# Performance work log

Measured on AMD Instinct MI355X. Metric: run time of the kernel, lower is better.

The kernel has to match this reference:

```python
import jax, jax.numpy as jnp
import numpy as np

IN_C, HID_C, OUT_C = 256, 512, 256
B, N = 8, 4096


def setup_inputs() -> dict:
    key = jax.random.key(0)
    ks = jax.random.split(key, 6)
    x = jax.random.normal(ks[0], (B, N, IN_C), dtype=jnp.float32)
    A = jax.random.uniform(ks[1], (B, N, N), dtype=jnp.float32)
    # Glorot-ish init for the two GCN layer weights + zero biases (PyG default bias=True)
    W1 = jax.random.normal(ks[2], (IN_C, HID_C), dtype=jnp.float32) * (1.0 / np.sqrt(IN_C))
    b1 = jnp.zeros((HID_C,), dtype=jnp.float32)
    W2 = jax.random.normal(ks[3], (HID_C, OUT_C), dtype=jnp.float32) * (1.0 / np.sqrt(HID_C))
    b2 = jnp.zeros((OUT_C,), dtype=jnp.float32)
    return {"x": x, "A": A, "W1": W1, "b1": b1, "W2": W2, "b2": b2}


def _gcn_norm(A):
    # dense equivalent of PyG gcn_norm with add_self_loops: A_hat = A + I,
    # norm = D^{-1/2} A_hat D^{-1/2}, with deg==0 -> 0 (inf guarded)
    A_hat = A + jnp.eye(A.shape[-1], dtype=A.dtype)  # [B,N,N]
    deg = A_hat.sum(axis=-1)                          # [B,N]
    d_inv_sqrt = jnp.where(deg > 0, jax.lax.rsqrt(jnp.maximum(deg, 1e-12)), 0.0)
    return d_inv_sqrt[:, :, None] * A_hat * d_inv_sqrt[:, None, :]


def reference(x, A, W1, b1, W2, b2):
    nrm = _gcn_norm(A)  # [B,N,N]
    # layer 1: out = A_hat_norm @ (x W1) + b1, then ReLU (dropout is identity in eval)
    h = jax.nn.relu(jnp.einsum('bij,bjh->bih', nrm, x @ W1) + b1)
    # layer 2
    out = jnp.einsum('bij,bjo->bio', nrm, h @ W2) + b2
    return out
```

## Files before the change

### kernel.cpp

```cpp
#include <hip/hip_runtime.h>
#include <stdint.h>

#define NN   4096
#define BATCH 8
#define IC   256
#define HC   512
#define OC   256
#define MTOT (BATCH * NN)

typedef float    f32x4 __attribute__((ext_vector_type(4)));
typedef __bf16   bf16x8 __attribute__((ext_vector_type(8)));
typedef uint16_t u16x8 __attribute__((ext_vector_type(8)));

__device__ __forceinline__ uint16_t f2b(float f) {
  union { float f; uint32_t u; } v; v.f = f;
  return (uint16_t)((v.u + 0x7FFFu + ((v.u >> 16) & 1u)) >> 16);
}

__global__ __launch_bounds__(256) void deg_kernel(const float* __restrict__ A,
                                                  float* __restrict__ dinv) {
  const int row = blockIdx.x;
  const float* ap = A + (size_t)row * NN;
  const int t = threadIdx.x;
  float s = 0.f;
#pragma unroll
  for (int i = 0; i < 4; ++i) {
    f32x4 v = *(const f32x4*)(ap + (t + 256 * i) * 4);
    s += v[0] + v[1] + v[2] + v[3];
  }
#pragma unroll
  for (int off = 32; off > 0; off >>= 1) s += __shfl_xor(s, off, 64);
  __shared__ float red[4];
  if ((t & 63) == 0) red[t >> 6] = s;
  __syncthreads();
  if (t == 0) {
    float deg = red[0] + red[1] + red[2] + red[3] + 1.0f;
    dinv[row] = 1.0f / sqrtf(deg);
  }
}

template<bool ABF16, int KTOT, int NC>
__global__ __launch_bounds__(256, 2) void xw_kernel(const void* __restrict__ Av,
                                                    const float* __restrict__ W,
                                                    const float* __restrict__ dinv,
                                                    uint16_t* __restrict__ Cout) {
  constexpr int BM = 128, BN = 128, BK = 64, LDT = 72;
  __shared__ uint16_t as_[BM * LDT];
  __shared__ uint16_t wt_[BN * LDT];
  const int t = threadIdx.x;
  const int m0 = blockIdx.x * BM;
  const int n0 = blockIdx.y * BN;
  const int lane = t & 63, wid = t >> 6;
  const int wm = wid >> 1, wn = wid & 1;
  f32x4 acc[4][4] = {};

  for (int kt = 0; kt < KTOT / BK; ++kt) {
    const int k0 = kt * BK;
    __syncthreads();
    if constexpr (!ABF16) {
      const float* Ap = (const float*)Av;
      const int c4 = t & 15, r0 = t >> 4;
#pragma unroll
      for (int i = 0; i < 8; ++i) {
        int r = r0 + 16 * i;
        f32x4 v = *(const f32x4*)(Ap + (size_t)(m0 + r) * KTOT + k0 + c4 * 4);
        uint32_t lo = f2b(v[0]) | ((uint32_t)f2b(v[1]) << 16);
        uint32_t hi = f2b(v[2]) | ((uint32_t)f2b(v[3]) << 16);
        *(uint2*)&as_[r * LDT + c4 * 4] = make_uint2(lo, hi);
      }
    } else {
      const uint16_t* Ap = (const uint16_t*)Av;
      const int c8 = t & 7, r0 = t >> 3;
#pragma unroll
      for (int i = 0; i < 4; ++i) {
        int r = r0 + 32 * i;
        u16x8 v = *(const u16x8*)(Ap + (size_t)(m0 + r) * KTOT + k0 + c8 * 8);
        *(u16x8*)&as_[r * LDT + c8 * 8] = v;
      }
    }
    {
      const int n4 = t & 31, kq = t >> 5;
#pragma unroll
      for (int i = 0; i < 8; ++i) {
        int k = kq + 8 * i;
        f32x4 v = *(const f32x4*)(W + (size_t)(k0 + k) * NC + n0 + n4 * 4);
        uint16_t hv[4] = { f2b(v[0]), f2b(v[1]), f2b(v[2]), f2b(v[3]) };
#pragma unroll
        for (int w = 0; w < 4; ++w) {
          int we = (w + n4) & 3;
          wt_[(n4 * 4 + we) * LDT + k] = hv[we];
        }
      }
    }
    __syncthreads();
#pragma unroll
    for (int kk = 0; kk < 2; ++kk) {
      bf16x8 bfr[4], afr[4];
#pragma unroll
      for (int fn = 0; fn < 4; ++fn)
        bfr[fn] = *(const bf16x8*)&wt_[(wn * 64 + fn * 16 + (lane & 15)) * LDT + kk * 32 + (lane >> 4) * 8];
#pragma unroll
      for (int fm = 0; fm < 4; ++fm)
        afr[fm] = *(const bf16x8*)&as_[(wm * 64 + fm * 16 + (lane & 15)) * LDT + kk * 32 + (lane >> 4) * 8];
#pragma unroll
      for (int fm = 0; fm < 4; ++fm)
#pragma unroll
        for (int fn = 0; fn < 4; ++fn)
          acc[fm][fn] = __builtin_amdgcn_mfma_f32_16x16x32_bf16(afr[fm], bfr[fn], acc[fm][fn], 0, 0, 0);
    }
  }
#pragma unroll
  for (int fm = 0; fm < 4; ++fm)
#pragma unroll
    for (int r = 0; r < 4; ++r) {
      int row = m0 + wm * 64 + fm * 16 + (lane >> 4) * 4 + r;
      float dv = dinv[row];
#pragma unroll
      for (int fn = 0; fn < 4; ++fn) {
        int col = n0 + wn * 64 + fn * 16 + (lane & 15);
        Cout[(size_t)row * NC + col] = f2b(acc[fm][fn][r] * dv);
      }
    }
}

template<int BN_, bool RELU>
__global__ __launch_bounds__(512, 2) void agg_kernel(const float* __restrict__ Amat,
                                                     const uint16_t* __restrict__ Vin,
                                                     const float* __restrict__ dinv,
                                                     const float* __restrict__ bias,
                                                     uint16_t* __restrict__ Hout,
                                                     float* __restrict__ Fout) {
  constexpr int BM = 128, BK = 64, LDT = 72;
  constexpr int FN = BN_ / 64;
  constexpr int WN = BN_ / 4;
  constexpr int CHN = BN_ / 8;
  constexpr int VT_TASKS = (64 * CHN) / 512;
  constexpr int NT = NN / BK;

  __shared__ uint16_t as_[BM * LDT];
  __shared__ uint16_t vt_[BN_ * LDT];

  const int t = threadIdx.x;
  const int bid = blockIdx.x;
  const int b = bid & 7;
  const int m0 = (bid >> 3) * BM;
  const int lane = t & 63, wid = t >> 6;
  const int wm = wid >> 2, wn = wid & 3;

  const float* Abase = Amat + ((size_t)b * NN + m0) * NN;
  const uint16_t* Vbase = Vin + (size_t)b * NN * BN_;

  const int ac4 = t & 15, ar0 = t >> 4;
  f32x4 apre[4];
  u16x8 vpre[VT_TASKS];

  auto load_tile = [&](int kt) {
    const int jj = kt * BK;
#pragma unroll
    for (int i = 0; i < 4; ++i)
      apre[i] = *(const f32x4*)(Abase + (size_t)(ar0 + 32 * i) * NN + jj + ac4 * 4);
#pragma unroll
    for (int i = 0; i < VT_TASKS; ++i) {
      int tt = i * 512 + t;
      int chunk = tt & (CHN - 1);
      int j = tt / CHN;
      vpre[i] = *(const u16x8*)(Vbase + (size_t)(jj + j) * BN_ + chunk * 8);
    }
  };

  load_tile(0);
  f32x4 acc[4][FN] = {};

  for (int kt = 0; kt < NT; ++kt) {
    const int j0 = kt * BK;
    __syncthreads();
#pragma unroll
    for (int i = 0; i < 4; ++i) {
      int r = ar0 + 32 * i;
      float f0 = apre[i][0], f1 = apre[i][1], f2c = apre[i][2], f3 = apre[i][3];
      int gc = j0 + ac4 * 4;
      int gr = m0 + r;
      if (gr == gc)          f0 += 1.0f;
      else if (gr == gc + 1) f1 += 1.0f;
      else if (gr == gc + 2) f2c += 1.0f;
      else if (gr == gc + 3) f3 += 1.0f;
      uint32_t lo = f2b(f0) | ((uint32_t)f2b(f1) << 16);
      uint32_t hi = f2b(f2c) | ((uint32_t)f2b(f3) << 16);
      *(uint2*)&as_[r * LDT + ac4 * 4] = make_uint2(lo, hi);
    }
#pragma unroll
    for (int i = 0; i < VT_TASKS; ++i) {
      int tt = i * 512 + t;
      int chunk = tt & (CHN - 1);
      int j = tt / CHN;
#pragma unroll
      for (int e = 0; e < 8; ++e) {
        int ee = (e + chunk) & 7;
        vt_[(chunk * 8 + ee) * LDT + j] = vpre[i][ee];
      }
    }
    __syncthreads();
    if (kt + 1 < NT) load_tile(kt + 1);
#pragma unroll
    for (int kk = 0; kk < 2; ++kk) {
      bf16x8 bfr[FN], afr[4];
#pragma unroll
      for (int fn = 0; fn < FN; ++fn)
        bfr[fn] = *(const bf16x8*)&vt_[(wn * WN + fn * 16 + (lane & 15)) * LDT + kk * 32 + (lane >> 4) * 8];
#pragma unroll
      for (int fm = 0; fm < 4; ++fm)
        afr[fm] = *(const bf16x8*)&as_[(wm * 64 + fm * 16 + (lane & 15)) * LDT + kk * 32 + (lane >> 4) * 8];
#pragma unroll
      for (int fm = 0; fm < 4; ++fm)
#pragma unroll
        for (int fn = 0; fn < FN; ++fn)
          acc[fm][fn] = __builtin_amdgcn_mfma_f32_16x16x32_bf16(afr[fm], bfr[fn], acc[fm][fn], 0, 0, 0);
    }
  }
#pragma unroll
  for (int fm = 0; fm < 4; ++fm)
#pragma unroll
    for (int r = 0; r < 4; ++r) {
      int rowl = wm * 64 + fm * 16 + (lane >> 4) * 4 + r;
      int grow = b * NN + m0 + rowl;
      float dv = dinv[grow];
#pragma unroll
      for (int fn = 0; fn < FN; ++fn) {
        int col = wn * WN + fn * 16 + (lane & 15);
        float v = acc[fm][fn][r] * dv + bias[col];
        if constexpr (RELU) {
          v = fmaxf(v, 0.0f);
          Hout[(size_t)grow * BN_ + col] = f2b(v);
        } else {
          Fout[(size_t)grow * BN_ + col] = v;
        }
      }
    }
}

extern "C" void kernel_launch(void* const* d_in, const int* in_sizes, int n_in,
                              void* d_out, int out_size, void* d_ws, size_t ws_size,
                              hipStream_t stream) {
  const float* x  = (const float*)d_in[0];
  const float* A  = (const float*)d_in[1];
  const float* W1 = (const float*)d_in[2];
  const float* b1 = (const float*)d_in[3];
  const float* W2 = (const float*)d_in[4];
  const float* b2 = (const float*)d_in[5];
  float* out = (float*)d_out;

  char* ws = (char*)d_ws;
  float*    dinv = (float*)ws;
  uint16_t* V1   = (uint16_t*)(ws + 131072);
  uint16_t* H    = (uint16_t*)(ws + 131072 + 33554432);
  uint16_t* V2   = (uint16_t*)(ws + 131072 + 2 * 33554432);

  deg_kernel<<<MTOT, 256, 0, stream>>>(A, dinv);
  xw_kernel<false, IC, HC><<<dim3(MTOT / 128, HC / 128), 256, 0, stream>>>(x, W1, dinv, V1);
  agg_kernel<HC, true><<<256, 512, 0, stream>>>(A, V1, dinv, b1, H, nullptr);
  xw_kernel<true, HC, OC><<<dim3(MTOT / 128, OC / 128), 256, 0, stream>>>(H, W2, dinv, V2);
  agg_kernel<OC, false><<<256, 512, 0, stream>>>(A, V2, dinv, b2, nullptr, out);
}
```

Baseline: 1.422 ms.

## Precompute normalized bf16 adjacency in tiled swizzled layout, load via global_load_lds

Adds a prep kernel that folds the self-loop and both D^-1/2 scalings into A once and stores it as bf16 in pre-tiled 64x64 XOR-swizzled blocks. The xw kernel now writes V transposed into the same tile layout, and the aggregation kernels stream both operands straight into LDS with global_load_lds, with no per-tile conversion or transpose. A is read in fp32 twice before this (degree plus prep) instead of three times, and each aggregation pass reads half the bytes of A. The cost is a 256 MB workspace and an extra pass that writes A. The aggregation tiles change to 64 rows by the full feature width, and the kernel no longer double-buffers its global loads.

```diff
diff --git a/kernel.cpp b/kernel.cpp
--- a/kernel.cpp
+++ b/kernel.cpp
@@ -6,15 +6,21 @@
 #define IC   256
 #define HC   512
 #define OC   256
-#define MTOT (BATCH * NN)
-
-typedef float    f32x4 __attribute__((ext_vector_type(4)));
+
+typedef float    f32x4  __attribute__((ext_vector_type(4)));
 typedef __bf16   bf16x8 __attribute__((ext_vector_type(8)));
-typedef uint16_t u16x8 __attribute__((ext_vector_type(8)));
+typedef uint16_t u16x8  __attribute__((ext_vector_type(8)));
+typedef uint16_t u16x4  __attribute__((ext_vector_type(4)));
 
 __device__ __forceinline__ uint16_t f2b(float f) {
   union { float f; uint32_t u; } v; v.f = f;
   return (uint16_t)((v.u + 0x7FFFu + ((v.u >> 16) & 1u)) >> 16);
+}
+
+__device__ __forceinline__ void gl_lds16(const void* g, void* l) {
+  __builtin_amdgcn_global_load_lds(
+      (const __attribute__((address_space(1))) uint32_t*)g,
+      (__attribute__((address_space(3))) uint32_t*)l, 16, 0, 0);
 }
 
 __global__ __launch_bounds__(256) void deg_kernel(const float* __restrict__ A,
@@ -39,23 +45,59 @@
   }
 }
 
+__global__ __launch_bounds__(256) void prep_kernel(const float* __restrict__ A,
+                                                   const float* __restrict__ dinv,
+                                                   uint16_t* __restrict__ Anorm) {
+  const int bid = blockIdx.x;
+  const int b = bid & 7, mt = (bid >> 3) & 63, kq = bid >> 9;
+  const int t = threadIdx.x;
+  const float* Ab = A + ((size_t)b * NN + mt * 64) * NN;
+  const float* dv = dinv + b * NN;
+  uint16_t* out = Anorm + ((size_t)(b * 64 + mt)) * 64 * 4096;
+  for (int kt = kq * 16; kt < kq * 16 + 16; ++kt) {
+#pragma unroll
+    for (int it = 0; it < 2; ++it) {
+      int tt = it * 256 + t;
+      int r = tt >> 3, g = tt & 7;
+      int i = mt * 64 + r;
+      int j0 = kt * 64 + g * 8;
+      const float* ap = Ab + (size_t)r * NN + j0;
+      f32x4 a0 = *(const f32x4*)ap;
+      f32x4 a1 = *(const f32x4*)(ap + 4);
+      float dvi = dv[i];
+      f32x4 d0 = *(const f32x4*)(dv + j0);
+      f32x4 d1 = *(const f32x4*)(dv + j0 + 4);
+      int dj = i - j0;
+      u16x8 o;
+#pragma unroll
+      for (int e = 0; e < 4; ++e) {
+        float v0 = (a0[e] + ((dj == e) ? 1.f : 0.f)) * dvi * d0[e];
+        float v1 = (a1[e] + ((dj == e + 4) ? 1.f : 0.f)) * dvi * d1[e];
+        o[e] = f2b(v0);
+        o[e + 4] = f2b(v1);
+      }
+      *(u16x8*)(out + ((size_t)kt * 64 + r) * 64 + (g ^ (r & 7)) * 8) = o;
+    }
+  }
+}
+
 template<bool ABF16, int KTOT, int NC>
 __global__ __launch_bounds__(256, 2) void xw_kernel(const void* __restrict__ Av,
                                                     const float* __restrict__ W,
-                                                    const float* __restrict__ dinv,
-                                                    uint16_t* __restrict__ Cout) {
-  constexpr int BM = 128, BN = 128, BK = 64, LDT = 72;
-  __shared__ uint16_t as_[BM * LDT];
-  __shared__ uint16_t wt_[BN * LDT];
-  const int t = threadIdx.x;
-  const int m0 = blockIdx.x * BM;
-  const int n0 = blockIdx.y * BN;
+                                                    uint16_t* __restrict__ Vt) {
+  constexpr int LDT = 72;
+  __shared__ uint16_t smem[18432];
+  uint16_t* as_ = smem;
+  uint16_t* wt_ = smem + 9216;
+  const int t = threadIdx.x;
+  const int m0 = blockIdx.x * 128;
+  const int n0 = blockIdx.y * 128;
   const int lane = t & 63, wid = t >> 6;
   const int wm = wid >> 1, wn = wid & 1;
   f32x4 acc[4][4] = {};
 
-  for (int kt = 0; kt < KTOT / BK; ++kt) {
-    const int k0 = kt * BK;
+  for (int kt = 0; kt < KTOT / 64; ++kt) {
+    const int k0 = kt * 64;
     __syncthreads();
     if constexpr (!ABF16) {
       const float* Ap = (const float*)Av;
@@ -109,111 +151,83 @@
           acc[fm][fn] = __builtin_amdgcn_mfma_f32_16x16x32_bf16(afr[fm], bfr[fn], acc[fm][fn], 0, 0, 0);
     }
   }
+  const int b = m0 >> 12;
+  const int kl0 = m0 & 4095;
+  __syncthreads();
+  uint16_t* lv = smem;
 #pragma unroll
   for (int fm = 0; fm < 4; ++fm)
 #pragma unroll
-    for (int r = 0; r < 4; ++r) {
-      int row = m0 + wm * 64 + fm * 16 + (lane >> 4) * 4 + r;
-      float dv = dinv[row];
-#pragma unroll
-      for (int fn = 0; fn < 4; ++fn) {
-        int col = n0 + wn * 64 + fn * 16 + (lane & 15);
-        Cout[(size_t)row * NC + col] = f2b(acc[fm][fn][r] * dv);
-      }
-    }
+    for (int fn = 0; fn < 4; ++fn) {
+      int nloc = wn * 64 + fn * 16 + (lane & 15);
+      int ml0  = wm * 64 + fm * 16 + (lane >> 4) * 4;
+      u16x4 pk;
+      pk[0] = f2b(acc[fm][fn][0]); pk[1] = f2b(acc[fm][fn][1]);
+      pk[2] = f2b(acc[fm][fn][2]); pk[3] = f2b(acc[fm][fn][3]);
+      *(u16x4*)&lv[nloc * 144 + ml0] = pk;
+    }
+  __syncthreads();
+#pragma unroll
+  for (int i = 0; i < 8; ++i) {
+    int nloc = (t >> 4) + 16 * i;
+    int ch = t & 15;
+    u16x8 v = *(const u16x8*)&lv[nloc * 144 + ch * 8];
+    int nglob = n0 + nloc;
+    int ktv = (kl0 >> 6) + (ch >> 3);
+    int s = (ch & 7) ^ (nglob & 7);
+    *(u16x8*)(Vt + (((size_t)b * 64 + ktv) * NC + nglob) * 64 + s * 8) = v;
+  }
 }
 
 template<int BN_, bool RELU>
-__global__ __launch_bounds__(512, 2) void agg_kernel(const float* __restrict__ Amat,
-                                                     const uint16_t* __restrict__ Vin,
-                                                     const float* __restrict__ dinv,
+__global__ __launch_bounds__(BN_, 4) void agg_kernel(const uint16_t* __restrict__ Anorm,
+                                                     const uint16_t* __restrict__ Vt,
                                                      const float* __restrict__ bias,
                                                      uint16_t* __restrict__ Hout,
                                                      float* __restrict__ Fout) {
-  constexpr int BM = 128, BK = 64, LDT = 72;
-  constexpr int FN = BN_ / 64;
-  constexpr int WN = BN_ / 4;
-  constexpr int CHN = BN_ / 8;
-  constexpr int VT_TASKS = (64 * CHN) / 512;
-  constexpr int NT = NN / BK;
-
-  __shared__ uint16_t as_[BM * LDT];
-  __shared__ uint16_t vt_[BN_ * LDT];
-
-  const int t = threadIdx.x;
+  constexpr int NWAVES = BN_ / 64;
+  __shared__ uint16_t as_[64 * 64];
+  __shared__ uint16_t vt_[BN_ * 64];
+  const int t = threadIdx.x;
+  const int lane = t & 63, wid = t >> 6;
   const int bid = blockIdx.x;
-  const int b = bid & 7;
-  const int m0 = (bid >> 3) * BM;
-  const int lane = t & 63, wid = t >> 6;
-  const int wm = wid >> 2, wn = wid & 3;
-
-  const float* Abase = Amat + ((size_t)b * NN + m0) * NN;
-  const uint16_t* Vbase = Vin + (size_t)b * NN * BN_;
-
-  const int ac4 = t & 15, ar0 = t >> 4;
-  f32x4 apre[4];
-  u16x8 vpre[VT_TASKS];
-
-  auto load_tile = [&](int kt) {
-    const int jj = kt * BK;
-#pragma unroll
-    for (int i = 0; i < 4; ++i)
-      apre[i] = *(const f32x4*)(Abase + (size_t)(ar0 + 32 * i) * NN + jj + ac4 * 4);
-#pragma unroll
-    for (int i = 0; i < VT_TASKS; ++i) {
-      int tt = i * 512 + t;
-      int chunk = tt & (CHN - 1);
-      int j = tt / CHN;
-      vpre[i] = *(const u16x8*)(Vbase + (size_t)(jj + j) * BN_ + chunk * 8);
-    }
-  };
-
-  load_tile(0);
-  f32x4 acc[4][FN] = {};
-
-  for (int kt = 0; kt < NT; ++kt) {
-    const int j0 = kt * BK;
-    __syncthreads();
-#pragma unroll
-    for (int i = 0; i < 4; ++i) {
-      int r = ar0 + 32 * i;
-      float f0 = apre[i][0], f1 = apre[i][1], f2c = apre[i][2], f3 = apre[i][3];
-      int gc = j0 + ac4 * 4;
-      int gr = m0 + r;
-      if (gr == gc)          f0 += 1.0f;
-      else if (gr == gc + 1) f1 += 1.0f;
-      else if (gr == gc + 2) f2c += 1.0f;
-      else if (gr == gc + 3) f3 += 1.0f;
-      uint32_t lo = f2b(f0) | ((uint32_t)f2b(f1) << 16);
-      uint32_t hi = f2b(f2c) | ((uint32_t)f2b(f3) << 16);
-      *(uint2*)&as_[r * LDT + ac4 * 4] = make_uint2(lo, hi);
-    }
-#pragma unroll
-    for (int i = 0; i < VT_TASKS; ++i) {
-      int tt = i * 512 + t;
-      int chunk = tt & (CHN - 1);
-      int j = tt / CHN;
-#pragma unroll
-      for (int e = 0; e < 8; ++e) {
-        int ee = (e + chunk) & 7;
-        vt_[(chunk * 8 + ee) * LDT + j] = vpre[i][ee];
-      }
-    }
-    __syncthreads();
-    if (kt + 1 < NT) load_tile(kt + 1);
+  const int b = bid & 7, mt = bid >> 3;
+  const int fr = lane & 15, c = lane >> 4;
+
+  const uint16_t* Abase = Anorm + ((size_t)(b * 64 + mt)) * 64 * 4096;
+  const uint16_t* Vbase = Vt + (size_t)b * 64 * BN_ * 64;
+
+  f32x4 acc[4][4] = {};
+
+  for (int kt = 0; kt < 64; ++kt) {
+    __syncthreads();
+    const uint16_t* At    = Abase + (size_t)kt * 4096;
+    const uint16_t* Vtile = Vbase + (size_t)kt * (BN_ * 64);
+    for (int ca = wid; ca < 8; ca += NWAVES)
+      gl_lds16(At + ca * 512 + lane * 8, &as_[ca * 512]);
+#pragma unroll
+    for (int i = 0; i < 8; ++i) {
+      int cv = wid * 8 + i;
+      gl_lds16(Vtile + cv * 512 + lane * 8, &vt_[cv * 512]);
+    }
+    __syncthreads();
 #pragma unroll
     for (int kk = 0; kk < 2; ++kk) {
-      bf16x8 bfr[FN], afr[4];
-#pragma unroll
-      for (int fn = 0; fn < FN; ++fn)
-        bfr[fn] = *(const bf16x8*)&vt_[(wn * WN + fn * 16 + (lane & 15)) * LDT + kk * 32 + (lane >> 4) * 8];
+      bf16x8 afr[4], bfr[4];
+#pragma unroll
+      for (int fm = 0; fm < 4; ++fm) {
+        int row = fm * 16 + fr;
+        afr[fm] = *(const bf16x8*)&as_[row * 64 + (((kk << 2) + c) ^ (row & 7)) * 8];
+      }
+#pragma unroll
+      for (int fn = 0; fn < 4; ++fn) {
+        int n = wid * 64 + fn * 16 + fr;
+        bfr[fn] = *(const bf16x8*)&vt_[n * 64 + (((kk << 2) + c) ^ (n & 7)) * 8];
+      }
 #pragma unroll
       for (int fm = 0; fm < 4; ++fm)
-        afr[fm] = *(const bf16x8*)&as_[(wm * 64 + fm * 16 + (lane & 15)) * LDT + kk * 32 + (lane >> 4) * 8];
-#pragma unroll
-      for (int fm = 0; fm < 4; ++fm)
-#pragma unroll
-        for (int fn = 0; fn < FN; ++fn)
+#pragma unroll
+        for (int fn = 0; fn < 4; ++fn)
           acc[fm][fn] = __builtin_amdgcn_mfma_f32_16x16x32_bf16(afr[fm], bfr[fn], acc[fm][fn], 0, 0, 0);
     }
   }
@@ -221,18 +235,15 @@
   for (int fm = 0; fm < 4; ++fm)
 #pragma unroll
     for (int r = 0; r < 4; ++r) {
-      int rowl = wm * 64 + fm * 16 + (lane >> 4) * 4 + r;
-      int grow = b * NN + m0 + rowl;
-      float dv = dinv[grow];
-#pragma unroll
-      for (int fn = 0; fn < FN; ++fn) {
-        int col = wn * WN + fn * 16 + (lane & 15);
-        float v = acc[fm][fn][r] * dv + bias[col];
+      size_t grow = (size_t)b * NN + mt * 64 + fm * 16 + (lane >> 4) * 4 + r;
+#pragma unroll
+      for (int fn = 0; fn < 4; ++fn) {
+        int col = wid * 64 + fn * 16 + fr;
+        float v = acc[fm][fn][r] + bias[col];
         if constexpr (RELU) {
-          v = fmaxf(v, 0.0f);
-          Hout[(size_t)grow * BN_ + col] = f2b(v);
+          Hout[grow * BN_ + col] = f2b(fmaxf(v, 0.f));
         } else {
-          Fout[(size_t)grow * BN_ + col] = v;
+          Fout[grow * BN_ + col] = v;
         }
       }
     }
@@ -250,14 +261,15 @@
   float* out = (float*)d_out;
 
   char* ws = (char*)d_ws;
-  float*    dinv = (float*)ws;
-  uint16_t* V1   = (uint16_t*)(ws + 131072);
-  uint16_t* H    = (uint16_t*)(ws + 131072 + 33554432);
-  uint16_t* V2   = (uint16_t*)(ws + 131072 + 2 * 33554432);
-
-  deg_kernel<<<MTOT, 256, 0, stream>>>(A, dinv);
-  xw_kernel<false, IC, HC><<<dim3(MTOT / 128, HC / 128), 256, 0, stream>>>(x, W1, dinv, V1);
-  agg_kernel<HC, true><<<256, 512, 0, stream>>>(A, V1, dinv, b1, H, nullptr);
-  xw_kernel<true, HC, OC><<<dim3(MTOT / 128, OC / 128), 256, 0, stream>>>(H, W2, dinv, V2);
-  agg_kernel<OC, false><<<256, 512, 0, stream>>>(A, V2, dinv, b2, nullptr, out);
-}
+  uint16_t* Anorm = (uint16_t*)ws;
+  float*    dinv  = (float*)(ws + 268435456);
+  uint16_t* Vt    = (uint16_t*)(ws + 268435456 + 131072);
+  uint16_t* H     = (uint16_t*)(ws + 268435456 + 131072 + 33554432);
+
+  deg_kernel<<<BATCH * NN, 256, 0, stream>>>(A, dinv);
+  prep_kernel<<<2048, 256, 0, stream>>>(A, dinv, Anorm);
+  xw_kernel<false, IC, HC><<<dim3(256, 4), 256, 0, stream>>>(x, W1, Vt);
+  agg_kernel<HC, true><<<512, 512, 0, stream>>>(Anorm, Vt, b1, H, nullptr);
+  xw_kernel<true, HC, OC><<<dim3(256, 2), 256, 0, stream>>>(H, W2, Vt);
+  agg_kernel<OC, false><<<512, 256, 0, stream>>>(Anorm, Vt, b2, nullptr, out);
+}
```

Result: faster. 1.203 ms (-15.4%).
